# Performance work log

Measured on AMD Instinct MI355X. Metric: run time of the kernel, lower is better.

The kernel has to match this reference:

```python
import jax, jax.numpy as jnp
import numpy as np

B, S, V, E, H, K = 32, 2048, 256, 512, 1024, 16


def setup_inputs() -> dict:
    key = jax.random.key(0)
    k0, k1, k2, k3, k4, k5 = jax.random.split(key, 6)
    return {
        "input_sequence": jax.random.randint(k0, (B, S), 0, V),
        "emb_table": jax.random.normal(k1, (V, E), dtype=jnp.float32),
        "conv_w": jax.random.normal(k2, (H, E, K), dtype=jnp.float32) * (1.0 / np.sqrt(E * K)),
        "conv_b": jnp.zeros((H,), dtype=jnp.float32),
        "lin_w": jax.random.normal(k4, (V, E + H), dtype=jnp.float32) * (1.0 / np.sqrt(E + H)),
        "lin_b": jnp.zeros((V,), dtype=jnp.float32),
    }


def reference(input_sequence, emb_table, conv_w, conv_b, lin_w, lin_b):
    # Embedding lookup: [B, S, E]
    emb = emb_table[input_sequence]
    # Conv1d over sequence with padding=K-1 (torch), then keep first S steps
    x = jnp.transpose(emb, (0, 2, 1))  # [B, E, S]
    y = jax.lax.conv_general_dilated(
        x, conv_w, window_strides=(1,), padding=[(K - 1, K - 1)],
        dimension_numbers=("NCH", "OIH", "NCH"))
    y = jax.nn.relu(y + conv_b[None, :, None])[:, :, :S]  # [B, H, S]
    conv_out = jnp.transpose(y, (0, 2, 1))  # [B, S, H]
    # PredNet: per-timestep cat + linear == one batched matmul over cat features
    feat = jnp.concatenate([emb, conv_out], axis=-1)  # [B, S, E+H]
    logits = jnp.einsum("bsf,vf->bsv", feat, lin_w) + lin_b
    return jax.nn.softmax(logits, axis=-1)
```

## Files before the change

kernel.cpp:

```cpp
#include <hip/hip_runtime.h>
#include <stdint.h>
#include <stddef.h>


typedef _Float16 f16;
typedef __attribute__((ext_vector_type(8))) _Float16 f16x8;
typedef __attribute__((ext_vector_type(4))) float f32x4;

#define SP 2063

__device__ __forceinline__ void gl2lds16(const void* g, void* l) {
  __builtin_amdgcn_global_load_lds((const __attribute__((address_space(1))) void*)g,
                                   (__attribute__((address_space(3))) void*)l, 16, 0, 0);
}

__global__ __launch_bounds__(256) void k_gather(const int* __restrict__ seq,
                                                const float* __restrict__ tab,
                                                f16* __restrict__ embp) {
  int row = blockIdx.x * 4 + (threadIdx.x >> 6);
  int lane = threadIdx.x & 63;
  int b = row / SP;
  int r = row - b * SP;
  f16* dst = embp + (size_t)row * 512 + lane * 8;
  if (r < 15) {
    f16x8 z = {(f16)0, (f16)0, (f16)0, (f16)0, (f16)0, (f16)0, (f16)0, (f16)0};
    *(f16x8*)dst = z;
  } else {
    int idx = seq[b * 2048 + (r - 15)];
    const float4* src = (const float4*)(tab + (size_t)idx * 512 + lane * 8);
    float4 v0 = src[0], v1 = src[1];
    f16x8 o;
    o[0] = (f16)v0.x; o[1] = (f16)v0.y; o[2] = (f16)v0.z; o[3] = (f16)v0.w;
    o[4] = (f16)v1.x; o[5] = (f16)v1.y; o[6] = (f16)v1.z; o[7] = (f16)v1.w;
    *(f16x8*)dst = o;
  }
}

__global__ __launch_bounds__(256) void k_twc(const float* __restrict__ cw,
                                             f16* __restrict__ wt2) {
  __shared__ f16 tile[8192];
  int h = blockIdx.x;
  const float4* src = (const float4*)(cw + (size_t)h * 8192);
#pragma unroll
  for (int i = 0; i < 8; ++i) {
    int o = i * 256 + threadIdx.x;
    float4 v = src[o];
    f16* d = tile + o * 4;
    d[0] = (f16)v.x; d[1] = (f16)v.y; d[2] = (f16)v.z; d[3] = (f16)v.w;
  }
  __syncthreads();
  int j = threadIdx.x >> 4, k = threadIdx.x & 15;
  f16* dst = wt2 + ((size_t)threadIdx.x * 1024 + h) * 32;
#pragma unroll
  for (int c8 = 0; c8 < 4; ++c8) {
    f16x8 v;
#pragma unroll
    for (int t = 0; t < 8; ++t) v[t] = tile[((j * 32 + c8 * 8 + t) << 4) | k];
    *(f16x8*)(dst + c8 * 8) = v;
  }
}

__global__ __launch_bounds__(256) void k_twl(const float* __restrict__ lw,
                                             f16* __restrict__ lt2) {
  int o = blockIdx.x * 256 + threadIdx.x;
  int f5 = o & 31;
  int v = (o >> 5) & 255;
  int kb = o >> 13;
  int f = (kb << 5) | f5;
  lt2[o] = (f16)lw[(size_t)v * 1536 + f];
}

__global__ __launch_bounds__(256) void k_conv(const f16* __restrict__ embp,
                                              const f16* __restrict__ wt2,
                                              const float* __restrict__ cb,
                                              f16* __restrict__ cout) {
  __shared__ __align__(16) f16 Asl[192 * 32];
  __shared__ __align__(16) f16 Bs[4 * 128 * 32];
  int bid = blockIdx.x;
  int x8 = bid & 7;
  int s = bid >> 3;
  int nb = s & 7;
  int mb = ((s >> 3) << 3) | x8;
  int n0 = nb << 7, m0 = mb << 7;
  int b = m0 >> 11, t0 = m0 & 2047;
  int tid = threadIdx.x, lane = tid & 63, wave = tid >> 6;
  int wr = wave >> 1, wc = wave & 1;
  int fr = lane & 15, q = lane >> 4;
  int prl = lane >> 2, pc = lane & 3;

  const f16* gAs[3];
#pragma unroll
  for (int c = 0; c < 3; ++c) {
    int pr = c * 64 + wave * 16 + prl;
    int clog = pc ^ ((pr >> 1) & 3);
    gAs[c] = embp + (size_t)(b * SP + t0 + pr) * 512 + clog * 8;
  }
  f16* lA0 = Asl + (wave * 16) * 32;
  const f16* gBs[2];
#pragma unroll
  for (int c = 0; c < 2; ++c) {
    int pr = c * 64 + wave * 16 + prl;
    int clog = pc ^ ((pr >> 1) & 3);
    gBs[c] = wt2 + (size_t)(n0 + pr) * 32 + clog * 8;
  }
  f16* lB0 = Bs + (wave * 16) * 32;

  int fqB = (q ^ ((fr >> 1) & 3)) << 3;

  f32x4 zero = {0.f, 0.f, 0.f, 0.f};
  f32x4 acc[4][4];
#pragma unroll
  for (int i = 0; i < 4; ++i)
#pragma unroll
    for (int jj = 0; jj < 4; ++jj) acc[i][jj] = zero;

  for (int j = 0; j < 16; ++j) {
#pragma unroll
    for (int c = 0; c < 3; ++c)
      gl2lds16(gAs[c] + j * 32, lA0 + c * 2048);
    for (int g = 0; g < 4; ++g) {
#pragma unroll
      for (int t = 0; t < 4; ++t) {
        size_t bOff = ((size_t)(j * 16 + g * 4 + t)) * 32768;
#pragma unroll
        for (int c = 0; c < 2; ++c)
          gl2lds16(gBs[c] + bOff, lB0 + t * 4096 + c * 2048);
      }
      __syncthreads();
#pragma unroll 2
      for (int t = 0; t < 4; ++t) {
        int k = g * 4 + t;
        int aswz = ((k + fr) >> 1) & 3;
        const f16* ap = Asl + (size_t)(k + wr * 64 + fr) * 32 + ((q ^ aswz) << 3);
        f16x8 af[4], bf[4];
#pragma unroll
        for (int i = 0; i < 4; ++i)
          af[i] = *(const f16x8*)(ap + i * 512);
#pragma unroll
        for (int jj = 0; jj < 4; ++jj)
          bf[jj] = *(const f16x8*)(Bs + t * 4096 + (wc * 64 + jj * 16 + fr) * 32 + fqB);
#pragma unroll
        for (int i = 0; i < 4; ++i)
#pragma unroll
          for (int jj = 0; jj < 4; ++jj)
            acc[i][jj] = __builtin_amdgcn_mfma_f32_16x16x32_f16(af[i], bf[jj], acc[i][jj], 0, 0, 0);
      }
      __syncthreads();
    }
  }
  int col = lane & 15, rq = (lane >> 4) << 2;
  int mbase = m0 + wr * 64 + rq;
  int nbase = n0 + wc * 64 + col;
#pragma unroll
  for (int jj = 0; jj < 4; ++jj) {
    int h = nbase + jj * 16;
    float bias = cb[h];
#pragma unroll
    for (int i = 0; i < 4; ++i) {
      int m = mbase + i * 16;
#pragma unroll
      for (int rg = 0; rg < 4; ++rg) {
        float v = acc[i][jj][rg] + bias;
        v = v > 0.f ? v : 0.f;
        cout[(size_t)(m + rg) * 1024 + h] = (f16)v;
      }
    }
  }
}

__global__ __launch_bounds__(256) void k_lin(const f16* __restrict__ embp,
                                             const f16* __restrict__ cout,
                                             const f16* __restrict__ lt2,
                                             const float* __restrict__ lb,
                                             float* __restrict__ out) {
  __shared__ __align__(16) char smem[32 * 261 * 4];
  __shared__ float pmax[4][32], psum[4][32], mrow[32], rinv[32];
  f16* As = (f16*)smem;
  f16* Bs = (f16*)(smem + 4096);
  float* Ls = (float*)smem;
  int m0 = blockIdx.x << 6;
  int b = m0 >> 11, t0 = m0 & 2047;
  int tid = threadIdx.x, lane = tid & 63, wave = tid >> 6;
  int sr = lane >> 2, sc = (lane & 3) << 3;
  const f16* gAe = embp + (size_t)(b * SP + 15 + t0 + wave * 16 + sr) * 512 + sc;
  const f16* gAc = cout + (size_t)(m0 + wave * 16 + sr) * 1024 + sc;
  f16* lA = As + wave * 512;
  int fr = lane & 15, fq = (lane >> 4) << 3;
  f32x4 zero = {0.f, 0.f, 0.f, 0.f};
  f32x4 acc[4][4];
#pragma unroll
  for (int i = 0; i < 4; ++i)
#pragma unroll
    for (int j = 0; j < 4; ++j) acc[i][j] = zero;

  for (int kb = 0; kb < 48; ++kb) {
    if (kb < 16) gl2lds16(gAe + kb * 32, lA);
    else         gl2lds16(gAc + (kb - 16) * 32, lA);
#pragma unroll
    for (int jj = 0; jj < 4; ++jj) {
      int c = wave * 4 + jj;
      gl2lds16(lt2 + (size_t)kb * 8192 + (c * 16 + sr) * 32 + sc, Bs + c * 512);
    }
    __syncthreads();
    f16x8 af[4], bf[4];
#pragma unroll
    for (int i = 0; i < 4; ++i)
      af[i] = *(const f16x8*)(As + (i * 16 + fr) * 32 + fq);
#pragma unroll
    for (int j = 0; j < 4; ++j)
      bf[j] = *(const f16x8*)(Bs + (wave * 64 + j * 16 + fr) * 32 + fq);
#pragma unroll
    for (int i = 0; i < 4; ++i)
#pragma unroll
      for (int j = 0; j < 4; ++j)
        acc[i][j] = __builtin_amdgcn_mfma_f32_16x16x32_f16(af[i], bf[j], acc[i][j], 0, 0, 0);
    __syncthreads();
  }

  int col = lane & 15, rq = (lane >> 4) << 2;
  for (int hf = 0; hf < 2; ++hf) {
    __syncthreads();
#pragma unroll
    for (int j = 0; j < 4; ++j) {
      int v = wave * 64 + j * 16 + col;
      float bias = lb[v];
#pragma unroll
      for (int i = 0; i < 2; ++i) {
        int rloc = i * 16 + rq;
        int ig = hf * 2 + i;
#pragma unroll
        for (int rg = 0; rg < 4; ++rg)
          Ls[(rloc + rg) * 261 + v] = acc[ig][j][rg] + bias;
      }
    }
    __syncthreads();
    if (tid < 128) {
      int r = tid & 31, qd = tid >> 5;
      const float* rowp = Ls + r * 261 + qd * 64;
      float pm = -1e30f;
#pragma unroll 8
      for (int c = 0; c < 64; ++c) pm = fmaxf(pm, rowp[c]);
      pmax[qd][r] = pm;
    }
    __syncthreads();
    if (tid < 32)
      mrow[tid] = fmaxf(fmaxf(pmax[0][tid], pmax[1][tid]), fmaxf(pmax[2][tid], pmax[3][tid]));
    __syncthreads();
    if (tid < 128) {
      int r = tid & 31, qd = tid >> 5;
      const float* rowp = Ls + r * 261 + qd * 64;
      float mr = mrow[r], ps = 0.f;
#pragma unroll 8
      for (int c = 0; c < 64; ++c) ps += __expf(rowp[c] - mr);
      psum[qd][r] = ps;
    }
    __syncthreads();
    if (tid < 32)
      rinv[tid] = 1.f / (psum[0][tid] + psum[1][tid] + psum[2][tid] + psum[3][tid]);
    __syncthreads();
    float* obase = out + (size_t)(m0 + hf * 32) * 256 + tid;
#pragma unroll 4
    for (int r = 0; r < 32; ++r)
      obase[(size_t)r * 256] = __expf(Ls[r * 261 + tid] - mrow[r]) * rinv[r];
  }
}

extern "C" void kernel_launch(void* const* d_in, const int* in_sizes, int n_in,
                              void* d_out, int out_size, void* d_ws, size_t ws_size,
                              hipStream_t stream) {
  const int*   seq = (const int*)d_in[0];
  const float* tab = (const float*)d_in[1];
  const float* cw  = (const float*)d_in[2];
  const float* cb  = (const float*)d_in[3];
  const float* lw  = (const float*)d_in[4];
  const float* lb  = (const float*)d_in[5];
  float* out = (float*)d_out;
  char* ws = (char*)d_ws;
  f16* embp = (f16*)(ws);
  f16* cout = (f16*)(ws + 67600384);
  f16* wt2  = (f16*)(ws + 201818112);
  f16* lt2  = (f16*)(ws + 218595328);

  hipLaunchKernelGGL(k_gather, dim3(16504), dim3(256), 0, stream, seq, tab, embp);
  hipLaunchKernelGGL(k_twc,    dim3(1024),  dim3(256), 0, stream, cw, wt2);
  hipLaunchKernelGGL(k_twl,    dim3(1536),  dim3(256), 0, stream, lw, lt2);
  hipLaunchKernelGGL(k_conv,   dim3(4096),  dim3(256), 0, stream, embp, wt2, cb, cout);
  hipLaunchKernelGGL(k_lin,    dim3(1024),  dim3(256), 0, stream, embp, cout, lt2, lb, out);
}
```

Baseline: 1.077 ms.

## Double-buffer conv A/B LDS tiles with software-pipelined global-to-LDS prefetch

```diff
diff --git a/kernel.cpp b/kernel.cpp
--- a/kernel.cpp
+++ b/kernel.cpp
@@ -74,8 +74,8 @@
                                               const f16* __restrict__ wt2,
                                               const float* __restrict__ cb,
                                               f16* __restrict__ cout) {
-  __shared__ __align__(16) f16 Asl[192 * 32];
-  __shared__ __align__(16) f16 Bs[4 * 128 * 32];
+  __shared__ __align__(16) f16 Asl[2 * 144 * 32];
+  __shared__ __align__(16) f16 Bsl[2 * 2 * 128 * 32];
   int bid = blockIdx.x;
   int x8 = bid & 7;
   int s = bid >> 3;
@@ -88,24 +88,44 @@
   int fr = lane & 15, q = lane >> 4;
   int prl = lane >> 2, pc = lane & 3;
 
-  const f16* gAs[3];
-#pragma unroll
-  for (int c = 0; c < 3; ++c) {
-    int pr = c * 64 + wave * 16 + prl;
-    int clog = pc ^ ((pr >> 1) & 3);
-    gAs[c] = embp + (size_t)(b * SP + t0 + pr) * 512 + clog * 8;
-  }
-  f16* lA0 = Asl + (wave * 16) * 32;
-  const f16* gBs[2];
+  const f16* gA[3];
 #pragma unroll
   for (int c = 0; c < 2; ++c) {
     int pr = c * 64 + wave * 16 + prl;
     int clog = pc ^ ((pr >> 1) & 3);
-    gBs[c] = wt2 + (size_t)(n0 + pr) * 32 + clog * 8;
-  }
-  f16* lB0 = Bs + (wave * 16) * 32;
+    gA[c] = embp + (size_t)(b * SP + t0 + pr) * 512 + clog * 8;
+  }
+  {
+    int pr = 128 + prl;
+    int clog = pc ^ ((pr >> 1) & 3);
+    gA[2] = embp + (size_t)(b * SP + t0 + pr) * 512 + clog * 8;
+  }
+  const f16* gB[2];
+#pragma unroll
+  for (int c = 0; c < 2; ++c) {
+    int pr = c * 64 + wave * 16 + prl;
+    int clog = pc ^ ((pr >> 1) & 3);
+    gB[c] = wt2 + (size_t)(n0 + pr) * 32 + clog * 8;
+  }
 
   int fqB = (q ^ ((fr >> 1) & 3)) << 3;
+
+  auto stage_a = [&](int jn) {
+    int jc = (jn & 1) * 4608;
+#pragma unroll
+    for (int c = 0; c < 2; ++c)
+      gl2lds16(gA[c] + jn * 32, Asl + jc + c * 2048 + wave * 512);
+    gl2lds16(gA[2] + jn * 32, Asl + jc + 4096);
+  };
+  auto stage_b = [&](int pn) {
+    int cn = (pn & 1) * 8192;
+#pragma unroll
+    for (int t = 0; t < 2; ++t)
+#pragma unroll
+      for (int c = 0; c < 2; ++c)
+        gl2lds16(gB[c] + (size_t)(2 * pn + t) * 32768,
+                 Bsl + cn + t * 4096 + c * 2048 + wave * 512);
+  };
 
   f32x4 zero = {0.f, 0.f, 0.f, 0.f};
   f32x4 acc[4][4];
@@ -114,40 +134,47 @@
 #pragma unroll
     for (int jj = 0; jj < 4; ++jj) acc[i][jj] = zero;
 
-  for (int j = 0; j < 16; ++j) {
-#pragma unroll
-    for (int c = 0; c < 3; ++c)
-      gl2lds16(gAs[c] + j * 32, lA0 + c * 2048);
-    for (int g = 0; g < 4; ++g) {
-#pragma unroll
-      for (int t = 0; t < 4; ++t) {
-        size_t bOff = ((size_t)(j * 16 + g * 4 + t)) * 32768;
-#pragma unroll
-        for (int c = 0; c < 2; ++c)
-          gl2lds16(gBs[c] + bOff, lB0 + t * 4096 + c * 2048);
-      }
-      __syncthreads();
-#pragma unroll 2
-      for (int t = 0; t < 4; ++t) {
-        int k = g * 4 + t;
-        int aswz = ((k + fr) >> 1) & 3;
-        const f16* ap = Asl + (size_t)(k + wr * 64 + fr) * 32 + ((q ^ aswz) << 3);
-        f16x8 af[4], bf[4];
-#pragma unroll
-        for (int i = 0; i < 4; ++i)
-          af[i] = *(const f16x8*)(ap + i * 512);
+  stage_a(0);
+  stage_b(0);
+
+#pragma unroll 1
+  for (int p = 0; p < 128; ++p) {
+    __builtin_amdgcn_s_barrier();
+    __builtin_amdgcn_sched_barrier(0);
+    if (p < 127) {
+      stage_b(p + 1);
+      if ((p & 7) == 7) stage_a((p >> 3) + 1);
+    }
+    if (p == 127)          asm volatile("s_waitcnt vmcnt(0)" ::: "memory");
+    else if ((p & 7) == 7) asm volatile("s_waitcnt vmcnt(7)" ::: "memory");
+    else                   asm volatile("s_waitcnt vmcnt(4)" ::: "memory");
+    __builtin_amdgcn_s_barrier();
+    __builtin_amdgcn_sched_barrier(0);
+
+    const f16* Ac = Asl + ((p >> 3) & 1) * 4608;
+    const f16* Bc = Bsl + (p & 1) * 8192;
+    __builtin_amdgcn_s_setprio(1);
+#pragma unroll
+    for (int t = 0; t < 2; ++t) {
+      int k = ((p & 7) << 1) + t;
+      int aswz = ((k + fr) >> 1) & 3;
+      const f16* ap = Ac + (size_t)(k + wr * 64 + fr) * 32 + ((q ^ aswz) << 3);
+      f16x8 af[4], bf[4];
+#pragma unroll
+      for (int i = 0; i < 4; ++i)
+        af[i] = *(const f16x8*)(ap + i * 512);
+#pragma unroll
+      for (int jj = 0; jj < 4; ++jj)
+        bf[jj] = *(const f16x8*)(Bc + t * 4096 + (wc * 64 + jj * 16 + fr) * 32 + fqB);
+#pragma unroll
+      for (int i = 0; i < 4; ++i)
 #pragma unroll
         for (int jj = 0; jj < 4; ++jj)
-          bf[jj] = *(const f16x8*)(Bs + t * 4096 + (wc * 64 + jj * 16 + fr) * 32 + fqB);
-#pragma unroll
-        for (int i = 0; i < 4; ++i)
-#pragma unroll
-          for (int jj = 0; jj < 4; ++jj)
-            acc[i][jj] = __builtin_amdgcn_mfma_f32_16x16x32_f16(af[i], bf[jj], acc[i][jj], 0, 0, 0);
-      }
-      __syncthreads();
-    }
-  }
+          acc[i][jj] = __builtin_amdgcn_mfma_f32_16x16x32_f16(af[i], bf[jj], acc[i][jj], 0, 0, 0);
+    }
+    __builtin_amdgcn_s_setprio(0);
+  }
+
   int col = lane & 15, rq = (lane >> 4) << 2;
   int mbase = m0 + wr * 64 + rq;
   int nbase = n0 + wc * 64 + col;
```

After: 1.113 ms. 3.3% more time.

## Load conv weights directly to registers with double buffering instead of LDS

Applied to the files above, without the earlier changes.

```diff
diff --git a/kernel.cpp b/kernel.cpp
--- a/kernel.cpp
+++ b/kernel.cpp
@@ -74,13 +74,10 @@
                                               const f16* __restrict__ wt2,
                                               const float* __restrict__ cb,
                                               f16* __restrict__ cout) {
-  __shared__ __align__(16) f16 Asl[192 * 32];
-  __shared__ __align__(16) f16 Bs[4 * 128 * 32];
+  __shared__ __align__(16) f16 Asl[144 * 32];
   int bid = blockIdx.x;
-  int x8 = bid & 7;
-  int s = bid >> 3;
-  int nb = s & 7;
-  int mb = ((s >> 3) << 3) | x8;
+  int nb = bid & 7;
+  int mb = bid >> 3;
   int n0 = nb << 7, m0 = mb << 7;
   int b = m0 >> 11, t0 = m0 & 2047;
   int tid = threadIdx.x, lane = tid & 63, wave = tid >> 6;
@@ -88,24 +85,20 @@
   int fr = lane & 15, q = lane >> 4;
   int prl = lane >> 2, pc = lane & 3;
 
-  const f16* gAs[3];
-#pragma unroll
-  for (int c = 0; c < 3; ++c) {
-    int pr = c * 64 + wave * 16 + prl;
-    int clog = pc ^ ((pr >> 1) & 3);
-    gAs[c] = embp + (size_t)(b * SP + t0 + pr) * 512 + clog * 8;
-  }
-  f16* lA0 = Asl + (wave * 16) * 32;
-  const f16* gBs[2];
+  const f16* gA[3];
 #pragma unroll
   for (int c = 0; c < 2; ++c) {
     int pr = c * 64 + wave * 16 + prl;
     int clog = pc ^ ((pr >> 1) & 3);
-    gBs[c] = wt2 + (size_t)(n0 + pr) * 32 + clog * 8;
-  }
-  f16* lB0 = Bs + (wave * 16) * 32;
-
-  int fqB = (q ^ ((fr >> 1) & 3)) << 3;
+    gA[c] = embp + (size_t)(b * SP + t0 + pr) * 512 + clog * 8;
+  }
+  {
+    int pr = 128 + prl;
+    int clog = pc ^ ((pr >> 1) & 3);
+    gA[2] = embp + (size_t)(b * SP + t0 + pr) * 512 + clog * 8;
+  }
+
+  const f16* gB = wt2 + (size_t)(n0 + wc * 64 + fr) * 32 + q * 8;
 
   f32x4 zero = {0.f, 0.f, 0.f, 0.f};
   f32x4 acc[4][4];
@@ -114,40 +107,62 @@
 #pragma unroll
     for (int jj = 0; jj < 4; ++jj) acc[i][jj] = zero;
 
+  f16x8 bA[4], bB[4];
   for (int j = 0; j < 16; ++j) {
-#pragma unroll
-    for (int c = 0; c < 3; ++c)
-      gl2lds16(gAs[c] + j * 32, lA0 + c * 2048);
-    for (int g = 0; g < 4; ++g) {
-#pragma unroll
-      for (int t = 0; t < 4; ++t) {
-        size_t bOff = ((size_t)(j * 16 + g * 4 + t)) * 32768;
-#pragma unroll
-        for (int c = 0; c < 2; ++c)
-          gl2lds16(gBs[c] + bOff, lB0 + t * 4096 + c * 2048);
-      }
-      __syncthreads();
-#pragma unroll 2
-      for (int t = 0; t < 4; ++t) {
-        int k = g * 4 + t;
+    if (j) __syncthreads();
+#pragma unroll
+    for (int c = 0; c < 2; ++c)
+      gl2lds16(gA[c] + j * 32, Asl + c * 2048 + wave * 512);
+    gl2lds16(gA[2] + j * 32, Asl + 4096);
+    {
+      const f16* p = gB + (size_t)(j * 16) * 32768;
+#pragma unroll
+      for (int jj = 0; jj < 4; ++jj) bA[jj] = *(const f16x8*)(p + jj * 512);
+    }
+    __syncthreads();
+
+#pragma unroll 1
+    for (int k2 = 0; k2 < 8; ++k2) {
+      int k = k2 * 2;
+      int jk = j * 16 + k;
+      {
+        const f16* p = gB + (size_t)(jk + 1) * 32768;
+#pragma unroll
+        for (int jj = 0; jj < 4; ++jj) bB[jj] = *(const f16x8*)(p + jj * 512);
+      }
+      {
         int aswz = ((k + fr) >> 1) & 3;
         const f16* ap = Asl + (size_t)(k + wr * 64 + fr) * 32 + ((q ^ aswz) << 3);
-        f16x8 af[4], bf[4];
+        f16x8 af[4];
+#pragma unroll
+        for (int i = 0; i < 4; ++i) af[i] = *(const f16x8*)(ap + i * 512);
 #pragma unroll
         for (int i = 0; i < 4; ++i)
-          af[i] = *(const f16x8*)(ap + i * 512);
-#pragma unroll
-        for (int jj = 0; jj < 4; ++jj)
-          bf[jj] = *(const f16x8*)(Bs + t * 4096 + (wc * 64 + jj * 16 + fr) * 32 + fqB);
+#pragma unroll
+          for (int jj = 0; jj < 4; ++jj)
+            acc[i][jj] = __builtin_amdgcn_mfma_f32_16x16x32_f16(af[i], bA[jj], acc[i][jj], 0, 0, 0);
+      }
+      if (k2 < 7) {
+        const f16* p = gB + (size_t)(jk + 2) * 32768;
+#pragma unroll
+        for (int jj = 0; jj < 4; ++jj) bA[jj] = *(const f16x8*)(p + jj * 512);
+      }
+      {
+        int k1 = k + 1;
+        int aswz = ((k1 + fr) >> 1) & 3;
+        const f16* ap = Asl + (size_t)(k1 + wr * 64 + fr) * 32 + ((q ^ aswz) << 3);
+        f16x8 af[4];
+#pragma unroll
+        for (int i = 0; i < 4; ++i) af[i] = *(const f16x8*)(ap + i * 512);
 #pragma unroll
         for (int i = 0; i < 4; ++i)
 #pragma unroll
           for (int jj = 0; jj < 4; ++jj)
-            acc[i][jj] = __builtin_amdgcn_mfma_f32_16x16x32_f16(af[i], bf[jj], acc[i][jj], 0, 0, 0);
-      }
-      __syncthreads();
-    }
-  }
+            acc[i][jj] = __builtin_amdgcn_mfma_f32_16x16x32_f16(af[i], bB[jj], acc[i][jj], 0, 0, 0);
+      }
+    }
+  }
+
   int col = lane & 15, rq = (lane >> 4) << 2;
   int mbase = m0 + wr * 64 + rq;
   int nbase = n0 + wc * 64 + col;
```

Result: slower. 1.262 ms (+17.2%).
